# Kernel optimization log

Measured on AMD Instinct MI355X. Metric: run time of the kernel, lower is better.

The kernel has to match this reference:

```python
import jax, jax.numpy as jnp
import numpy as np

B, S = 1, 2048
H, KV, D = 32, 8, 128          # query heads, kv heads, head_size
G = H // KV                     # num_queries_per_kv (GQA group size)
SCALE = 1.0 / float(np.sqrt(D))


def setup_inputs() -> dict:
    key = jax.random.key(0)
    k1, k2, k3 = jax.random.split(key, 3)
    slopes = jnp.asarray(2.0 ** (-8.0 * np.arange(1, H + 1) / H), dtype=jnp.float32)
    return {
        "query": jax.random.normal(k1, (B, S, H * D), dtype=jnp.float32),
        "key": jax.random.normal(k2, (B, S, KV * D), dtype=jnp.float32),
        "value": jax.random.normal(k3, (B, S, KV * D), dtype=jnp.float32),
        "alibi_slopes": slopes,
    }


def reference(query, key, value, alibi_slopes):
    b, s, _ = query.shape
    # [B,S,H*D] -> [B,KV,G,S,D] (GQA unflatten of query heads into kv groups)
    q = query.reshape(b, s, KV, G, D).transpose(0, 2, 3, 1, 4)
    k = key.reshape(b, s, KV, D).transpose(0, 2, 1, 3)      # [B,KV,S,D]
    v = value.reshape(b, s, KV, D).transpose(0, 2, 1, 3)    # [B,KV,S,D]

    # _make_alibi_bias: bias[i,j] = (j - i) * slope_h, then unflatten heads to (KV, G)
    pos = jnp.arange(s)
    rel = (pos[None, :] - pos[:, None]).astype(query.dtype)         # [S,S]
    bias = alibi_slopes[:, None, None] * rel                        # [H,S,S]
    causal = jnp.where(pos[None, :] > pos[:, None], -jnp.inf, 0.0).astype(query.dtype)
    bias = (bias + causal).reshape(KV, G, s, s)                     # [KV,G,S,S]

    # scaled QK^T + bias, softmax, AV (non-fused prompt_attention path)
    scores = jnp.einsum('bkgsd,bktd->bkgst', q * SCALE, k) + bias   # [B,KV,G,S,S]
    probs = jax.nn.softmax(scores, axis=-1)
    out = jnp.einsum('bkgst,bktd->bkgsd', probs, v)                 # [B,KV,G,S,D]
    # flatten (KV,G) -> H and back to [B,S,H*D]
    return out.transpose(0, 3, 1, 2, 4).reshape(b, s, H * D)
```

## Files before the change

### kernel.cpp

```cpp
#include <hip/hip_runtime.h>
#include <hip/hip_bf16.h>

#define S_LEN 2048
#define NHEADS 32
#define NKV 8
#define HD 128
#define QK_SCALE 0.08838834764831845f
#define LOG2E 1.4426950408889634f
#define QK_SCALE2 (QK_SCALE * LOG2E)
#define DTHR 11.5416f

#define BQ 64
#define BK 32
#define NQT (S_LEN / BQ)
#define QSTR (NHEADS * HD)
#define KSTR (NKV * HD)

#define K_STRIDE 136
#define VT_STRIDE 40
#define P_STRIDE 40

typedef __attribute__((ext_vector_type(8))) short bf16x8;
typedef __attribute__((ext_vector_type(4))) float f32x4;
typedef __attribute__((ext_vector_type(4))) unsigned u32x4;
typedef __attribute__((ext_vector_type(2))) unsigned u32x2;

__device__ inline unsigned cvt_pk_bf16(float lo, float hi) {
    unsigned r;
    asm("v_cvt_pk_bf16_f32 %0, %1, %2" : "=v"(r) : "v"(lo), "v"(hi));
    return r;
}
__device__ inline bf16x8 as_bf16x8(u32x4 v) {
    union { u32x4 u; bf16x8 b; } c; c.u = v; return c.b;
}

__global__ __launch_bounds__(256) void prep_k(const float* __restrict__ K,
                                              short* __restrict__ Kbf) {
    int g = blockIdx.x * 256 + threadIdx.x;
    int chunk = g & 15, kvh = (g >> 4) & 7, s = g >> 7;
    const float* in = K + (size_t)s * KSTR + kvh * HD + chunk * 8;
    f32x4 a = *(const f32x4*)in;
    f32x4 b = *(const f32x4*)(in + 4);
    u32x4 t;
    t[0] = cvt_pk_bf16(a[0], a[1]); t[1] = cvt_pk_bf16(a[2], a[3]);
    t[2] = cvt_pk_bf16(b[0], b[1]); t[3] = cvt_pk_bf16(b[2], b[3]);
    *(u32x4*)(Kbf + ((size_t)kvh * S_LEN + s) * HD + chunk * 8) = t;
}

__global__ __launch_bounds__(256) void prep_v(const float* __restrict__ V,
                                              short* __restrict__ Vtb) {
    __shared__ short Ts[64][72];
    int b = blockIdx.x;
    int sb = b & 31, db = (b >> 5) & 1, kvh = b >> 6;
    int t = threadIdx.x, r = t >> 2, c0 = (t & 3) * 16;

    const float* in = V + (size_t)(sb * 64 + r) * KSTR + kvh * HD + db * 64 + c0;
    f32x4 a0 = *(const f32x4*)in,        a1 = *(const f32x4*)(in + 4);
    f32x4 a2 = *(const f32x4*)(in + 8),  a3 = *(const f32x4*)(in + 12);
    u32x4 t0;
    t0[0] = cvt_pk_bf16(a0[0], a0[1]); t0[1] = cvt_pk_bf16(a0[2], a0[3]);
    t0[2] = cvt_pk_bf16(a1[0], a1[1]); t0[3] = cvt_pk_bf16(a1[2], a1[3]);
    *(u32x4*)&Ts[r][c0] = t0;
    t0[0] = cvt_pk_bf16(a2[0], a2[1]); t0[1] = cvt_pk_bf16(a2[2], a2[3]);
    t0[2] = cvt_pk_bf16(a3[0], a3[1]); t0[3] = cvt_pk_bf16(a3[2], a3[3]);
    *(u32x4*)&Ts[r][c0 + 8] = t0;
    __syncthreads();

    alignas(16) short tmp[16];
    #pragma unroll
    for (int j = 0; j < 16; ++j) tmp[j] = Ts[c0 + j][r];
    short* dst = Vtb + ((size_t)(kvh * HD + db * 64 + r)) * S_LEN + sb * 64 + c0;
    *(u32x4*)dst       = *(u32x4*)&tmp[0];
    *(u32x4*)(dst + 8) = *(u32x4*)&tmp[8];
}

__global__ __launch_bounds__(256) void attn_fwd(
    const float* __restrict__ Q, const short* __restrict__ Kbf,
    const short* __restrict__ Vtb, const float* __restrict__ SL,
    float* __restrict__ O)
{
    const int bx   = blockIdx.x;
    const int h    = bx & (NHEADS - 1);
    const int qt   = (NQT - 1) - (bx >> 5);
    const int kvh  = h >> 2;
    const float slope  = SL[h];
    const float slope2 = slope * LOG2E;

    const int tid  = threadIdx.x;
    const int lane = tid & 63;
    const int w    = tid >> 6;
    const int l16  = lane & 15;
    const int lq   = lane >> 4;

    __shared__ short Ks[2][BK * K_STRIDE];
    __shared__ short VTs[2][HD * VT_STRIDE];
    __shared__ short Ps[4][16 * P_STRIDE];

    const int qrow0 = qt * BQ + w * 16;
    const int q     = qrow0 + l16;

    bf16x8 qf[4];
    {
        const float* qp = Q + (size_t)q * QSTR + h * HD + lq * 8;
        #pragma unroll
        for (int d0 = 0; d0 < 4; ++d0) {
            f32x4 a = *(const f32x4*)(qp + d0 * 32);
            f32x4 b = *(const f32x4*)(qp + d0 * 32 + 4);
            u32x4 t;
            t[0] = cvt_pk_bf16(a[0] * QK_SCALE2, a[1] * QK_SCALE2);
            t[1] = cvt_pk_bf16(a[2] * QK_SCALE2, a[3] * QK_SCALE2);
            t[2] = cvt_pk_bf16(b[0] * QK_SCALE2, b[1] * QK_SCALE2);
            t[3] = cvt_pk_bf16(b[2] * QK_SCALE2, b[3] * QK_SCALE2);
            qf[d0] = as_bf16x8(t);
        }
    }
    bf16x8 onesf;
    #pragma unroll
    for (int j = 0; j < 8; ++j) onesf[j] = (short)0x3f80;

    f32x4 acc[8];
    #pragma unroll
    for (int t = 0; t < 8; ++t) acc[t] = (f32x4){0.f, 0.f, 0.f, 0.f};
    f32x4 sums = (f32x4){0.f, 0.f, 0.f, 0.f};
    float m_ = -1e30f;

    const int kv_end = qt * BQ + BQ;
    int kb_start = 0;
    {
        float th = (float)(qt * BQ) - 31.0f - 45.0f / slope;
        int t = (int)floorf(th);
        kb_start = (t < 0) ? 0 : (((t >> 5) + 1) << 5);
    }

    const int sr  = tid >> 4, scc = tid & 15;
    const int vd  = tid & 127, vrb = (tid >> 7) * 8;
    const short* Kst = Kbf + (size_t)kvh * S_LEN * HD + scc * 8;
    const short* Vst = Vtb + (size_t)(kvh * HD + vd) * S_LEN;

    u32x4 kreg[2], vreg[2];

    auto load_regs = [&](int kb) {
        #pragma unroll
        for (int s = 0; s < 2; ++s)
            kreg[s] = *(const u32x4*)(Kst + (size_t)(kb + sr + s * 16) * HD);
        #pragma unroll
        for (int s = 0; s < 2; ++s)
            vreg[s] = *(const u32x4*)(Vst + kb + vrb + s * 16);
    };

    auto store_tile = [&](int b) {
        #pragma unroll
        for (int s = 0; s < 2; ++s)
            *(u32x4*)&Ks[b][(sr + s * 16) * K_STRIDE + scc * 8] = kreg[s];
        #pragma unroll
        for (int s = 0; s < 2; ++s)
            *(u32x4*)&VTs[b][vd * VT_STRIDE + vrb + s * 16] = vreg[s];
    };

    load_regs(kb_start);
    store_tile(0);
    int cur = 0;

    for (int kb = kb_start; kb < kv_end; kb += BK) {
        asm volatile("s_waitcnt lgkmcnt(0)\n\ts_barrier" ::: "memory");

        const bool has_next = (kb + BK) < kv_end;
        if (has_next) load_regs(kb + BK);

        const bool live = (kb <= qrow0 + 15) &&
                          (slope * (float)(qrow0 - kb - 31) < 45.0f);
        if (live) {
            const short* Kc = &Ks[cur][0];
            const short* Vc = &VTs[cur][0];

            f32x4 sc0 = (f32x4){0.f,0.f,0.f,0.f};
            f32x4 sc1 = (f32x4){0.f,0.f,0.f,0.f};
            #pragma unroll
            for (int d0 = 0; d0 < 4; ++d0) {
                bf16x8 kf0 = *(const bf16x8*)&Kc[l16 * K_STRIDE + d0 * 32 + lq * 8];
                bf16x8 kf1 = *(const bf16x8*)&Kc[(16 + l16) * K_STRIDE + d0 * 32 + lq * 8];
                sc0 = __builtin_amdgcn_mfma_f32_16x16x32_bf16(kf0, qf[d0], sc0, 0, 0, 0);
                sc1 = __builtin_amdgcn_mfma_f32_16x16x32_bf16(kf1, qf[d0], sc1, 0, 0, 0);
            }

            const int kq0 = kb + 4 * lq - q;
            float s[8];
            #pragma unroll
            for (int i = 0; i < 4; ++i) {
                int d0i = kq0 + i, d1i = kq0 + 16 + i;
                float b0 = __builtin_fmaf(slope2, (float)d0i, sc0[i]);
                float b1 = __builtin_fmaf(slope2, (float)d1i, sc1[i]);
                s[i]     = (d0i > 0) ? -1e30f : b0;
                s[i + 4] = (d1i > 0) ? -1e30f : b1;
            }

            float lm = fmaxf(fmaxf(fmaxf(s[0], s[1]), fmaxf(s[2], s[3])),
                             fmaxf(fmaxf(s[4], s[5]), fmaxf(s[6], s[7])));
            if (__any(lm > m_ + DTHR)) {
                float rm = lm;
                rm = fmaxf(rm, __shfl_xor(rm, 16));
                rm = fmaxf(rm, __shfl_xor(rm, 32));
                if (rm > m_ + DTHR) {
                    float alpha = exp2f(m_ - rm);
                    m_ = rm;
                    sums[0] *= alpha; sums[1] *= alpha;
                    sums[2] *= alpha; sums[3] *= alpha;
                    #pragma unroll
                    for (int t = 0; t < 8; ++t) {
                        acc[t][0] *= alpha; acc[t][1] *= alpha;
                        acc[t][2] *= alpha; acc[t][3] *= alpha;
                    }
                }
            }

            float p[8];
            #pragma unroll
            for (int j = 0; j < 8; ++j) p[j] = exp2f(s[j] - m_);

            u32x2 pa, pb;
            pa[0] = cvt_pk_bf16(p[0], p[1]); pa[1] = cvt_pk_bf16(p[2], p[3]);
            pb[0] = cvt_pk_bf16(p[4], p[5]); pb[1] = cvt_pk_bf16(p[6], p[7]);

            short* PsW = &Ps[w][0];
            *(u32x2*)&PsW[l16 * P_STRIDE + 4 * lq]      = pa;
            *(u32x2*)&PsW[l16 * P_STRIDE + 16 + 4 * lq] = pb;
            asm volatile("s_waitcnt lgkmcnt(0)" ::: "memory");
            bf16x8 pf = *(const bf16x8*)&PsW[l16 * P_STRIDE + lq * 8];

            sums = __builtin_amdgcn_mfma_f32_16x16x32_bf16(onesf, pf, sums, 0, 0, 0);

            #pragma unroll
            for (int nt = 0; nt < 8; ++nt) {
                bf16x8 vf = *(const bf16x8*)&Vc[(nt * 16 + l16) * VT_STRIDE + lq * 8];
                acc[nt] = __builtin_amdgcn_mfma_f32_16x16x32_bf16(vf, pf, acc[nt], 0, 0, 0);
            }
        }

        if (has_next) store_tile(cur ^ 1);
        cur ^= 1;
    }

    {
        float rl = 1.0f / sums[0];
        float* op = O + (size_t)q * QSTR + h * HD + 4 * lq;
        #pragma unroll
        for (int nt = 0; nt < 8; ++nt) {
            f32x4 o = acc[nt];
            o[0] *= rl; o[1] *= rl; o[2] *= rl; o[3] *= rl;
            *(f32x4*)(op + nt * 16) = o;
        }
    }
}

extern "C" void kernel_launch(void* const* d_in, const int* in_sizes, int n_in,
                              void* d_out, int out_size, void* d_ws, size_t ws_size,
                              hipStream_t stream) {
    const float* Q  = (const float*)d_in[0];
    const float* K  = (const float*)d_in[1];
    const float* V  = (const float*)d_in[2];
    const float* SL = (const float*)d_in[3];
    float* O = (float*)d_out;

    short* Kbf = (short*)d_ws;
    short* Vtb = (short*)d_ws + (size_t)NKV * S_LEN * HD;

    prep_k<<<dim3(1024), dim3(256), 0, stream>>>(K, Kbf);
    prep_v<<<dim3(512),  dim3(256), 0, stream>>>(V, Vtb);
    attn_fwd<<<dim3(NQT * NHEADS), dim3(256), 0, stream>>>(Q, Kbf, Vtb, SL, O);
}
```

Before: 90.64 us.

## Merge K/V prep kernels, remap blocks by KV head, add MFMA setprio

Merges the separate K-convert and V-transpose prep kernels into one launch that branches on block index, removing one kernel launch and its gap. Remaps the attention grid so consecutive blocks walk across KV heads, with the four query heads of a group placed 8 blocks apart, which changes how blocks sharing K/V tiles land on CUs and in L2. Raises wave priority around the MFMA sections so matrix-core issue is favoured over other waves. The __syncthreads inside the V branch is now in a divergent-by-block path, which is safe because the condition is uniform per block.

```diff
diff --git a/kernel.cpp b/kernel.cpp
--- a/kernel.cpp
+++ b/kernel.cpp
@@ -34,44 +34,46 @@
     union { u32x4 u; bf16x8 b; } c; c.u = v; return c.b;
 }
 
-__global__ __launch_bounds__(256) void prep_k(const float* __restrict__ K,
-                                              short* __restrict__ Kbf) {
-    int g = blockIdx.x * 256 + threadIdx.x;
-    int chunk = g & 15, kvh = (g >> 4) & 7, s = g >> 7;
-    const float* in = K + (size_t)s * KSTR + kvh * HD + chunk * 8;
-    f32x4 a = *(const f32x4*)in;
-    f32x4 b = *(const f32x4*)(in + 4);
-    u32x4 t;
-    t[0] = cvt_pk_bf16(a[0], a[1]); t[1] = cvt_pk_bf16(a[2], a[3]);
-    t[2] = cvt_pk_bf16(b[0], b[1]); t[3] = cvt_pk_bf16(b[2], b[3]);
-    *(u32x4*)(Kbf + ((size_t)kvh * S_LEN + s) * HD + chunk * 8) = t;
-}
-
-__global__ __launch_bounds__(256) void prep_v(const float* __restrict__ V,
-                                              short* __restrict__ Vtb) {
+__global__ __launch_bounds__(256) void prep_kv(
+    const float* __restrict__ K, const float* __restrict__ V,
+    short* __restrict__ Kbf, short* __restrict__ Vtb)
+{
     __shared__ short Ts[64][72];
-    int b = blockIdx.x;
-    int sb = b & 31, db = (b >> 5) & 1, kvh = b >> 6;
-    int t = threadIdx.x, r = t >> 2, c0 = (t & 3) * 16;
-
-    const float* in = V + (size_t)(sb * 64 + r) * KSTR + kvh * HD + db * 64 + c0;
-    f32x4 a0 = *(const f32x4*)in,        a1 = *(const f32x4*)(in + 4);
-    f32x4 a2 = *(const f32x4*)(in + 8),  a3 = *(const f32x4*)(in + 12);
-    u32x4 t0;
-    t0[0] = cvt_pk_bf16(a0[0], a0[1]); t0[1] = cvt_pk_bf16(a0[2], a0[3]);
-    t0[2] = cvt_pk_bf16(a1[0], a1[1]); t0[3] = cvt_pk_bf16(a1[2], a1[3]);
-    *(u32x4*)&Ts[r][c0] = t0;
-    t0[0] = cvt_pk_bf16(a2[0], a2[1]); t0[1] = cvt_pk_bf16(a2[2], a2[3]);
-    t0[2] = cvt_pk_bf16(a3[0], a3[1]); t0[3] = cvt_pk_bf16(a3[2], a3[3]);
-    *(u32x4*)&Ts[r][c0 + 8] = t0;
-    __syncthreads();
-
-    alignas(16) short tmp[16];
-    #pragma unroll
-    for (int j = 0; j < 16; ++j) tmp[j] = Ts[c0 + j][r];
-    short* dst = Vtb + ((size_t)(kvh * HD + db * 64 + r)) * S_LEN + sb * 64 + c0;
-    *(u32x4*)dst       = *(u32x4*)&tmp[0];
-    *(u32x4*)(dst + 8) = *(u32x4*)&tmp[8];
+    const int b = blockIdx.x;
+    if (b < 1024) {
+        int g = b * 256 + threadIdx.x;
+        int chunk = g & 15, kvh = (g >> 4) & 7, s = g >> 7;
+        const float* in = K + (size_t)s * KSTR + kvh * HD + chunk * 8;
+        f32x4 a = *(const f32x4*)in;
+        f32x4 c = *(const f32x4*)(in + 4);
+        u32x4 t;
+        t[0] = cvt_pk_bf16(a[0], a[1]); t[1] = cvt_pk_bf16(a[2], a[3]);
+        t[2] = cvt_pk_bf16(c[0], c[1]); t[3] = cvt_pk_bf16(c[2], c[3]);
+        *(u32x4*)(Kbf + ((size_t)kvh * S_LEN + s) * HD + chunk * 8) = t;
+    } else {
+        int bv = b - 1024;
+        int sb = bv & 31, db = (bv >> 5) & 1, kvh = bv >> 6;
+        int t = threadIdx.x, r = t >> 2, c0 = (t & 3) * 16;
+
+        const float* in = V + (size_t)(sb * 64 + r) * KSTR + kvh * HD + db * 64 + c0;
+        f32x4 a0 = *(const f32x4*)in,        a1 = *(const f32x4*)(in + 4);
+        f32x4 a2 = *(const f32x4*)(in + 8),  a3 = *(const f32x4*)(in + 12);
+        u32x4 t0;
+        t0[0] = cvt_pk_bf16(a0[0], a0[1]); t0[1] = cvt_pk_bf16(a0[2], a0[3]);
+        t0[2] = cvt_pk_bf16(a1[0], a1[1]); t0[3] = cvt_pk_bf16(a1[2], a1[3]);
+        *(u32x4*)&Ts[r][c0] = t0;
+        t0[0] = cvt_pk_bf16(a2[0], a2[1]); t0[1] = cvt_pk_bf16(a2[2], a2[3]);
+        t0[2] = cvt_pk_bf16(a3[0], a3[1]); t0[3] = cvt_pk_bf16(a3[2], a3[3]);
+        *(u32x4*)&Ts[r][c0 + 8] = t0;
+        __syncthreads();
+
+        alignas(16) short tmp[16];
+        #pragma unroll
+        for (int j = 0; j < 16; ++j) tmp[j] = Ts[c0 + j][r];
+        short* dst = Vtb + ((size_t)(kvh * HD + db * 64 + r)) * S_LEN + sb * 64 + c0;
+        *(u32x4*)dst       = *(u32x4*)&tmp[0];
+        *(u32x4*)(dst + 8) = *(u32x4*)&tmp[8];
+    }
 }
 
 __global__ __launch_bounds__(256) void attn_fwd(
@@ -79,10 +81,11 @@
     const short* __restrict__ Vtb, const float* __restrict__ SL,
     float* __restrict__ O)
 {
-    const int bx   = blockIdx.x;
-    const int h    = bx & (NHEADS - 1);
-    const int qt   = (NQT - 1) - (bx >> 5);
-    const int kvh  = h >> 2;
+    const int bx = blockIdx.x;
+    const int kvh = bx & 7;
+    const int i   = bx >> 3;
+    const int qt  = (NQT - 1) - (i >> 2);
+    const int h   = kvh * 4 + (i & 3);
     const float slope  = SL[h];
     const float slope2 = slope * LOG2E;
 
@@ -175,6 +178,7 @@
 
             f32x4 sc0 = (f32x4){0.f,0.f,0.f,0.f};
             f32x4 sc1 = (f32x4){0.f,0.f,0.f,0.f};
+            __builtin_amdgcn_s_setprio(1);
             #pragma unroll
             for (int d0 = 0; d0 < 4; ++d0) {
                 bf16x8 kf0 = *(const bf16x8*)&Kc[l16 * K_STRIDE + d0 * 32 + lq * 8];
@@ -182,16 +186,17 @@
                 sc0 = __builtin_amdgcn_mfma_f32_16x16x32_bf16(kf0, qf[d0], sc0, 0, 0, 0);
                 sc1 = __builtin_amdgcn_mfma_f32_16x16x32_bf16(kf1, qf[d0], sc1, 0, 0, 0);
             }
+            __builtin_amdgcn_s_setprio(0);
 
             const int kq0 = kb + 4 * lq - q;
             float s[8];
             #pragma unroll
-            for (int i = 0; i < 4; ++i) {
-                int d0i = kq0 + i, d1i = kq0 + 16 + i;
-                float b0 = __builtin_fmaf(slope2, (float)d0i, sc0[i]);
-                float b1 = __builtin_fmaf(slope2, (float)d1i, sc1[i]);
-                s[i]     = (d0i > 0) ? -1e30f : b0;
-                s[i + 4] = (d1i > 0) ? -1e30f : b1;
+            for (int i2 = 0; i2 < 4; ++i2) {
+                int d0i = kq0 + i2, d1i = kq0 + 16 + i2;
+                float b0 = __builtin_fmaf(slope2, (float)d0i, sc0[i2]);
+                float b1 = __builtin_fmaf(slope2, (float)d1i, sc1[i2]);
+                s[i2]     = (d0i > 0) ? -1e30f : b0;
+                s[i2 + 4] = (d1i > 0) ? -1e30f : b1;
             }
 
             float lm = fmaxf(fmaxf(fmaxf(s[0], s[1]), fmaxf(s[2], s[3])),
@@ -227,13 +232,14 @@
             asm volatile("s_waitcnt lgkmcnt(0)" ::: "memory");
             bf16x8 pf = *(const bf16x8*)&PsW[l16 * P_STRIDE + lq * 8];
 
+            __builtin_amdgcn_s_setprio(1);
             sums = __builtin_amdgcn_mfma_f32_16x16x32_bf16(onesf, pf, sums, 0, 0, 0);
-
             #pragma unroll
             for (int nt = 0; nt < 8; ++nt) {
                 bf16x8 vf = *(const bf16x8*)&Vc[(nt * 16 + l16) * VT_STRIDE + lq * 8];
                 acc[nt] = __builtin_amdgcn_mfma_f32_16x16x32_bf16(vf, pf, acc[nt], 0, 0, 0);
             }
+            __builtin_amdgcn_s_setprio(0);
         }
 
         if (has_next) store_tile(cur ^ 1);
@@ -264,7 +270,6 @@
     short* Kbf = (short*)d_ws;
     short* Vtb = (short*)d_ws + (size_t)NKV * S_LEN * HD;
 
-    prep_k<<<dim3(1024), dim3(256), 0, stream>>>(K, Kbf);
-    prep_v<<<dim3(512),  dim3(256), 0, stream>>>(V, Vtb);
+    prep_kv<<<dim3(1536), dim3(256), 0, stream>>>(K, V, Kbf, Vtb);
     attn_fwd<<<dim3(NQT * NHEADS), dim3(256), 0, stream>>>(Q, Kbf, Vtb, SL, O);
 }
```

After: 91.50 us. Within noise of the previous version (+1.0%).
